# Kernel tuning notes

Hardware: AMD Instinct MI355X
Metric: run time of the kernel (lower is better)

The kernel has to match this reference:

```python
import jax, jax.numpy as jnp
import numpy as np

INPUT_DIM, HIDDEN, OUTPUT_DIM, NUM_LAYERS = 512, 128, 96, 5
BATCH, SEQ = 64, 512


def _gru_layer(x_seq, w_ih, w_hh, b_ih, b_hh):
    """Single GRU layer, PyTorch gate conventions. x_seq: [B,T,I] -> [B,T,H]."""
    B = x_seq.shape[0]
    H = w_hh.shape[1]
    # Precompute input-to-hidden gates for all timesteps: [B,T,3H]
    gx = jnp.einsum('bti,gi->btg', x_seq, w_ih) + b_ih

    def step(h, gx_t):
        gh = h @ w_hh.T + b_hh                      # [B,3H]
        xr, xz, xn = jnp.split(gx_t, 3, axis=-1)
        hr, hz, hn = jnp.split(gh, 3, axis=-1)
        r = jax.nn.sigmoid(xr + hr)
        z = jax.nn.sigmoid(xz + hz)
        n = jnp.tanh(xn + r * hn)
        h_new = (1.0 - z) * n + z * h
        return h_new, h_new

    h0 = jnp.zeros((B, H), x_seq.dtype)
    _, hs = jax.lax.scan(step, h0, jnp.swapaxes(gx, 0, 1))  # [T,B,H]
    return jnp.swapaxes(hs, 0, 1)                           # [B,T,H]


def setup_inputs() -> dict:
    key = jax.random.key(0)
    ks = jax.random.split(key, 8)
    s = 1.0 / np.sqrt(HIDDEN)  # torch default uniform init bound
    u = lambda k, shape: jax.random.uniform(k, shape, jnp.float32, -s, s)
    return {
        'x': jax.random.normal(ks[0], (BATCH, SEQ, INPUT_DIM), jnp.float32),
        'w_ih0': u(ks[1], (3 * HIDDEN, INPUT_DIM)),
        'w_ih_rest': u(ks[2], (NUM_LAYERS - 1, 3 * HIDDEN, HIDDEN)),
        'w_hh': u(ks[3], (NUM_LAYERS, 3 * HIDDEN, HIDDEN)),
        'b_ih': u(ks[4], (NUM_LAYERS, 3 * HIDDEN)),
        'b_hh': u(ks[5], (NUM_LAYERS, 3 * HIDDEN)),
        'fc_w': u(ks[6], (OUTPUT_DIM, HIDDEN)),
        'fc_b': u(ks[7], (OUTPUT_DIM,)),
    }


def reference(x, w_ih0, w_ih_rest, w_hh, b_ih, b_hh, fc_w, fc_b):
    h = _gru_layer(x, w_ih0, w_hh[0], b_ih[0], b_hh[0])
    for l in range(1, NUM_LAYERS):
        h = _gru_layer(h, w_ih_rest[l - 1], w_hh[l], b_ih[l], b_hh[l])
    # final linear on last timestep: [B,H] -> [B,OUTPUT_DIM]
    return h[:, -1, :] @ fc_w.T + fc_b
```

## Files before the change

kernel.cpp:

```cpp
#include <hip/hip_runtime.h>
#include <hip/hip_bf16.h>

#define BATCH   64
#define SEQ     512
#define IN0     512
#define HID     128
#define G3      384
#define NLAY    5
#define CHUNK   8

typedef _Float16 f16x8 __attribute__((ext_vector_type(8)));
typedef float    f32x4 __attribute__((ext_vector_type(4)));

static __device__ __forceinline__ float sigf(float x) {
    return __builtin_amdgcn_rcpf(1.f + __expf(-x));
}
static __device__ __forceinline__ float tanh_fast(float x) {
    const float e = __expf(-2.f * fabsf(x));
    return copysignf((1.f - e) * __builtin_amdgcn_rcpf(1.f + e), x);
}

__global__ __launch_bounds__(256) void gemm_gx(const float* __restrict__ A,
                                               const float* __restrict__ W,
                                               const float* __restrict__ bias,
                                               float* __restrict__ gx)
{
    __shared__ __align__(16) _Float16 As[64][40];
    __shared__ __align__(16) _Float16 Bs[64][40];

    const int tid  = threadIdx.x;
    const int lane = tid & 63;
    const int wv   = tid >> 6;
    const int n16  = lane & 15;
    const int quad = lane >> 4;
    const int row0 = blockIdx.x * 64;
    const int col0 = blockIdx.y * 64;
    const int r    = tid >> 2;
    const int kc   = (tid & 3) * 8;

    f32x4 acc[4];
    #pragma unroll
    for (int nt = 0; nt < 4; nt++) acc[nt] = (f32x4){0.f, 0.f, 0.f, 0.f};

    for (int k0 = 0; k0 < IN0; k0 += 32) {
        {
            const float* Ap = A + (size_t)(row0 + r) * IN0 + k0 + kc;
            float4 a0 = *(const float4*)(Ap);
            float4 a1 = *(const float4*)(Ap + 4);
            f16x8 v;
            v[0] = (_Float16)a0.x; v[1] = (_Float16)a0.y; v[2] = (_Float16)a0.z; v[3] = (_Float16)a0.w;
            v[4] = (_Float16)a1.x; v[5] = (_Float16)a1.y; v[6] = (_Float16)a1.z; v[7] = (_Float16)a1.w;
            *(f16x8*)&As[r][kc] = v;
        }
        {
            const float* Wp = W + (size_t)(col0 + r) * IN0 + k0 + kc;
            float4 b0 = *(const float4*)(Wp);
            float4 b1 = *(const float4*)(Wp + 4);
            f16x8 v;
            v[0] = (_Float16)b0.x; v[1] = (_Float16)b0.y; v[2] = (_Float16)b0.z; v[3] = (_Float16)b0.w;
            v[4] = (_Float16)b1.x; v[5] = (_Float16)b1.y; v[6] = (_Float16)b1.z; v[7] = (_Float16)b1.w;
            *(f16x8*)&Bs[r][kc] = v;
        }
        __syncthreads();

        const f16x8 af = *(const f16x8*)&As[wv * 16 + n16][quad * 8];
        #pragma unroll
        for (int nt = 0; nt < 4; nt++) {
            const f16x8 bfr = *(const f16x8*)&Bs[nt * 16 + n16][quad * 8];
            acc[nt] = __builtin_amdgcn_mfma_f32_16x16x32_f16(af, bfr, acc[nt], 0, 0, 0);
        }
        __syncthreads();
    }

    #pragma unroll
    for (int nt = 0; nt < 4; nt++) {
        const int col = col0 + nt * 16 + n16;
        const float bb = bias[col];
        #pragma unroll
        for (int r4 = 0; r4 < 4; r4++) {
            const int row = row0 + wv * 16 + quad * 4 + r4;
            gx[(size_t)row * G3 + col] = acc[nt][r4] + bb;
        }
    }
}

__global__ __launch_bounds__(512, 2) void gru_pipeline(
    const float* __restrict__ gx0,
    const float* __restrict__ w_ih_rest,
    const float* __restrict__ w_hh,
    const float* __restrict__ b_ih,
    const float* __restrict__ b_hh,
    _Float16* __restrict__ hmid,
    float* __restrict__ hlast,
    int* __restrict__ flags)
{
    const int l    = blockIdx.x >> 2;
    const int g    = blockIdx.x & 3;
    const int bm0  = g * 16;
    const int tid  = threadIdx.x;
    const int lane = tid & 63;
    const int n16  = lane & 15;
    const int quad = lane >> 4;
    const int wv   = tid >> 6;
    const int j    = wv * 16 + n16;

    __shared__ __align__(16) _Float16 hA[2][16][136];
    __shared__ int barcnt;

    f16x8 bf[3][4];
    {
        const float* wb = w_hh + (size_t)l * G3 * HID;
        #pragma unroll
        for (int tau = 0; tau < 3; tau++)
            #pragma unroll
            for (int kc = 0; kc < 4; kc++) {
                const float* wp = wb + (size_t)(tau * 128 + j) * HID + kc * 32 + quad * 8;
                f16x8 v;
                #pragma unroll
                for (int i = 0; i < 8; i++) v[i] = (_Float16)wp[i];
                bf[tau][kc] = v;
            }
    }
    f16x8 bi[3][4];
    if (l > 0) {
        const float* wb = w_ih_rest + (size_t)(l - 1) * G3 * HID;
        #pragma unroll
        for (int tau = 0; tau < 3; tau++)
            #pragma unroll
            for (int kc = 0; kc < 4; kc++) {
                const float* wp = wb + (size_t)(tau * 128 + j) * HID + kc * 32 + quad * 8;
                f16x8 v;
                #pragma unroll
                for (int i = 0; i < 8; i++) v[i] = (_Float16)wp[i];
                bi[tau][kc] = v;
            }
    }
    const float bcr = b_hh[l * G3 + j]       + ((l > 0) ? b_ih[l * G3 + j]       : 0.f);
    const float bcz = b_hh[l * G3 + j + 128] + ((l > 0) ? b_ih[l * G3 + j + 128] : 0.f);
    const float bcn = b_hh[l * G3 + j + 256];
    const float bxn = (l > 0) ? b_ih[l * G3 + j + 256] : 0.f;

    for (int i = tid; i < 2 * 16 * 136; i += 512) ((_Float16*)hA)[i] = (_Float16)0.f;
    float vhp[4] = {0.f, 0.f, 0.f, 0.f};
    if (tid == 0) barcnt = 0;

    const float* pR[4];
    float xr[4], xz[4], xn[4];
    if (l == 0) {
        #pragma unroll
        for (int r = 0; r < 4; r++) {
            pR[r] = gx0 + (size_t)(bm0 + quad * 4 + r) * SEQ * G3 + j;
            xr[r] = pR[r][0]; xz[r] = pR[r][128]; xn[r] = pR[r][256];
            pR[r] += G3;
        }
    }

    const _Float16* hprev = (l > 0) ? hmid + (size_t)((l - 1) * 4 + g) * SEQ * 2048 : (const _Float16*)nullptr;
    _Float16*       hpub  = (l < 4) ? hmid + (size_t)(l * 4 + g) * SEQ * 2048 : (_Float16*)nullptr;
    int*       dstflag = (l < 4) ? &flags[l * 4 + g] : (int*)nullptr;
    const int* srcflag = (l > 0) ? &flags[(l - 1) * 4 + g] : (const int*)nullptr;

    _Float16* hw = (l < 4) ? hpub + quad * 4 * 128 + j : (_Float16*)nullptr;

    f16x8 ap[4];
    const int hoff = n16 * 128 + quad * 8;

    __syncthreads();

    volatile int* bc = &barcnt;
    int btarget = 0;

    for (int c = 0; c < SEQ / CHUNK; c++) {
        const int t0 = c * CHUNK;

        if (l > 0) {
            const int need = t0 + CHUNK;
            int v = __hip_atomic_load(srcflag, __ATOMIC_RELAXED, __HIP_MEMORY_SCOPE_AGENT);
            while (v < need) {
                __builtin_amdgcn_s_sleep(2);
                v = __hip_atomic_load(srcflag, __ATOMIC_RELAXED, __HIP_MEMORY_SCOPE_AGENT);
            }
            (void)__hip_atomic_load(srcflag, __ATOMIC_ACQUIRE, __HIP_MEMORY_SCOPE_AGENT);
            __asm__ volatile("" ::: "memory");
            const _Float16* hp = hprev + (size_t)t0 * 2048 + hoff;
            #pragma unroll
            for (int kc = 0; kc < 4; kc++) ap[kc] = *(const f16x8*)(hp + kc * 32);
        }

        #pragma unroll
        for (int i = 0; i < CHUNK; i++) {
            const int t = t0 + i;

            __asm__ volatile("" ::: "memory");
            if (lane == 0) atomicAdd(&barcnt, 1);
            btarget += 8;
            while (*bc < btarget) { __builtin_amdgcn_s_sleep(1); }
            __asm__ volatile("" ::: "memory");

            const int buf = t & 1;
            f16x8 af[4];
            #pragma unroll
            for (int kc = 0; kc < 4; kc++)
                af[kc] = *(const f16x8*)&hA[buf][n16][kc * 32 + quad * 8];

            f32x4 ai0 = {0.f,0.f,0.f,0.f}, ai1 = ai0, ai2 = ai0;
            if (l > 0) {
                #pragma unroll
                for (int kc = 0; kc < 4; kc++) {
                    ai0 = __builtin_amdgcn_mfma_f32_16x16x32_f16(ap[kc], bi[0][kc], ai0, 0, 0, 0);
                    ai1 = __builtin_amdgcn_mfma_f32_16x16x32_f16(ap[kc], bi[1][kc], ai1, 0, 0, 0);
                    ai2 = __builtin_amdgcn_mfma_f32_16x16x32_f16(ap[kc], bi[2][kc], ai2, 0, 0, 0);
                }
            }
            float nr[4], nz[4], nn[4];
            if (l == 0) {
                #pragma unroll
                for (int r = 0; r < 4; r++) {
                    nr[r] = pR[r][0]; nz[r] = pR[r][128]; nn[r] = pR[r][256];
                }
                if (t + 1 < SEQ) {
                    #pragma unroll
                    for (int r = 0; r < 4; r++) pR[r] += G3;
                }
            }

            f32x4 ah0 = {0.f,0.f,0.f,0.f}, ah1 = ah0, ah2 = ah0;
            #pragma unroll
            for (int kc = 0; kc < 4; kc++) {
                ah0 = __builtin_amdgcn_mfma_f32_16x16x32_f16(af[kc], bf[0][kc], ah0, 0, 0, 0);
                ah1 = __builtin_amdgcn_mfma_f32_16x16x32_f16(af[kc], bf[1][kc], ah1, 0, 0, 0);
                ah2 = __builtin_amdgcn_mfma_f32_16x16x32_f16(af[kc], bf[2][kc], ah2, 0, 0, 0);
            }

            const int nbuf = buf ^ 1;
            #pragma unroll
            for (int r = 0; r < 4; r++) {
                const float sxr = (l == 0) ? xr[r] : ai0[r];
                const float sxz = (l == 0) ? xz[r] : ai1[r];
                const float sxn = ((l == 0) ? xn[r] : ai2[r]) + bxn;
                const float rg  = sigf(sxr + ah0[r] + bcr);
                const float zg  = sigf(sxz + ah1[r] + bcz);
                const float th  = tanh_fast(sxn + rg * (ah2[r] + bcn));
                const float hnew = fmaf(zg, vhp[r] - th, th);
                vhp[r] = hnew;
                hA[nbuf][quad * 4 + r][j] = (_Float16)hnew;
                if (l < 4) hw[r * 128] = (_Float16)hnew;
                if (l == 4 && t == SEQ - 1)
                    hlast[(bm0 + quad * 4 + r) * 128 + j] = hnew;
            }
            if (l < 4) hw += 2048;

            if (l == 0) {
                #pragma unroll
                for (int r = 0; r < 4; r++) { xr[r] = nr[r]; xz[r] = nz[r]; xn[r] = nn[r]; }
            }

            if (l > 0 && i < CHUNK - 1) {
                const _Float16* hp = hprev + (size_t)(t + 1) * 2048 + hoff;
                #pragma unroll
                for (int kc = 0; kc < 4; kc++) ap[kc] = *(const f16x8*)(hp + kc * 32);
            }
        }

        __syncthreads();
        if (l < 4 && tid == 0)
            __hip_atomic_store(dstflag, t0 + CHUNK, __ATOMIC_RELEASE, __HIP_MEMORY_SCOPE_AGENT);
    }
}

__global__ __launch_bounds__(128) void fc_kernel(const float* __restrict__ hlast,
                                                 const float* __restrict__ fc_w,
                                                 const float* __restrict__ fc_b,
                                                 float* __restrict__ out)
{
    const int b = blockIdx.x;
    const int o = threadIdx.x;
    if (o < 96) {
        const float* h = hlast + (size_t)b * HID;
        const float* wrow = fc_w + o * HID;
        float acc = fc_b[o];
        #pragma unroll 4
        for (int k = 0; k < HID; k++) acc = fmaf(h[k], wrow[k], acc);
        out[b * 96 + o] = acc;
    }
}

extern "C" void kernel_launch(void* const* d_in, const int* in_sizes, int n_in,
                              void* d_out, int out_size, void* d_ws, size_t ws_size,
                              hipStream_t stream)
{
    const float* x         = (const float*)d_in[0];
    const float* w_ih0     = (const float*)d_in[1];
    const float* w_ih_rest = (const float*)d_in[2];
    const float* w_hh      = (const float*)d_in[3];
    const float* b_ih      = (const float*)d_in[4];
    const float* b_hh      = (const float*)d_in[5];
    const float* fc_w      = (const float*)d_in[6];
    const float* fc_b      = (const float*)d_in[7];
    float* out = (float*)d_out;

    int*      flags = (int*)d_ws;
    float*    gxbuf = (float*)((char*)d_ws + 256);
    _Float16* hmid  = (_Float16*)((char*)d_ws + 256 + 50331648);
    float*    hlast = (float*)((char*)d_ws + 256 + 50331648 + 33554432);

    hipMemsetAsync(d_ws, 0, 256, stream);

    const dim3 gemmGrid(512, 6);
    gemm_gx<<<gemmGrid, 256, 0, stream>>>(x, w_ih0, b_ih, gxbuf);

    gru_pipeline<<<NLAY * 4, 512, 0, stream>>>(gxbuf, w_ih_rest, w_hh, b_ih, b_hh,
                                               hmid, hlast, flags);

    fc_kernel<<<BATCH, 128, 0, stream>>>(hlast, fc_w, fc_b, out);
}
```

Baseline: 983.9 us.

## Fuse layer-0 input GEMM into GRU kernel with per-chunk readiness counters

Merges the separate input-projection GEMM into the persistent GRU pipeline launch. Extra blocks compute gx tiles ordered by time chunk and batch group, then bump per-(group, time-chunk) counters. Layer-0 recurrent blocks spin on those counters before consuming each 128-step chunk. The goal is to overlap the GEMM with the start of the recurrence and drop one launch boundary. In exchange it relies on block scheduling order for forward progress, and the stores use relaxed ordering with no release fence before the counter increment.

```diff
diff --git a/kernel.cpp b/kernel.cpp
--- a/kernel.cpp
+++ b/kernel.cpp
@@ -20,88 +20,93 @@
     return copysignf((1.f - e) * __builtin_amdgcn_rcpf(1.f + e), x);
 }
 
-__global__ __launch_bounds__(256) void gemm_gx(const float* __restrict__ A,
-                                               const float* __restrict__ W,
-                                               const float* __restrict__ bias,
-                                               float* __restrict__ gx)
-{
-    __shared__ __align__(16) _Float16 As[64][40];
-    __shared__ __align__(16) _Float16 Bs[64][40];
-
-    const int tid  = threadIdx.x;
-    const int lane = tid & 63;
-    const int wv   = tid >> 6;
-    const int n16  = lane & 15;
-    const int quad = lane >> 4;
-    const int row0 = blockIdx.x * 64;
-    const int col0 = blockIdx.y * 64;
-    const int r    = tid >> 2;
-    const int kc   = (tid & 3) * 8;
-
-    f32x4 acc[4];
-    #pragma unroll
-    for (int nt = 0; nt < 4; nt++) acc[nt] = (f32x4){0.f, 0.f, 0.f, 0.f};
-
-    for (int k0 = 0; k0 < IN0; k0 += 32) {
-        {
-            const float* Ap = A + (size_t)(row0 + r) * IN0 + k0 + kc;
-            float4 a0 = *(const float4*)(Ap);
-            float4 a1 = *(const float4*)(Ap + 4);
-            f16x8 v;
-            v[0] = (_Float16)a0.x; v[1] = (_Float16)a0.y; v[2] = (_Float16)a0.z; v[3] = (_Float16)a0.w;
-            v[4] = (_Float16)a1.x; v[5] = (_Float16)a1.y; v[6] = (_Float16)a1.z; v[7] = (_Float16)a1.w;
-            *(f16x8*)&As[r][kc] = v;
-        }
-        {
-            const float* Wp = W + (size_t)(col0 + r) * IN0 + k0 + kc;
-            float4 b0 = *(const float4*)(Wp);
-            float4 b1 = *(const float4*)(Wp + 4);
-            f16x8 v;
-            v[0] = (_Float16)b0.x; v[1] = (_Float16)b0.y; v[2] = (_Float16)b0.z; v[3] = (_Float16)b0.w;
-            v[4] = (_Float16)b1.x; v[5] = (_Float16)b1.y; v[6] = (_Float16)b1.z; v[7] = (_Float16)b1.w;
-            *(f16x8*)&Bs[r][kc] = v;
-        }
-        __syncthreads();
-
-        const f16x8 af = *(const f16x8*)&As[wv * 16 + n16][quad * 8];
-        #pragma unroll
-        for (int nt = 0; nt < 4; nt++) {
-            const f16x8 bfr = *(const f16x8*)&Bs[nt * 16 + n16][quad * 8];
-            acc[nt] = __builtin_amdgcn_mfma_f32_16x16x32_f16(af, bfr, acc[nt], 0, 0, 0);
-        }
-        __syncthreads();
-    }
-
-    #pragma unroll
-    for (int nt = 0; nt < 4; nt++) {
-        const int col = col0 + nt * 16 + n16;
-        const float bb = bias[col];
-        #pragma unroll
-        for (int r4 = 0; r4 < 4; r4++) {
-            const int row = row0 + wv * 16 + quad * 4 + r4;
-            gx[(size_t)row * G3 + col] = acc[nt][r4] + bb;
-        }
-    }
-}
-
-__global__ __launch_bounds__(512, 2) void gru_pipeline(
-    const float* __restrict__ gx0,
+__global__ __launch_bounds__(512, 2) void gru_fused(
+    const float* __restrict__ x,
+    const float* __restrict__ w_ih0,
     const float* __restrict__ w_ih_rest,
     const float* __restrict__ w_hh,
     const float* __restrict__ b_ih,
     const float* __restrict__ b_hh,
+    float* __restrict__ gx0,
     _Float16* __restrict__ hmid,
     float* __restrict__ hlast,
-    int* __restrict__ flags)
+    int* __restrict__ flags,
+    int* __restrict__ gxcnt)
 {
-    const int l    = blockIdx.x >> 2;
-    const int g    = blockIdx.x & 3;
-    const int bm0  = g * 16;
     const int tid  = threadIdx.x;
     const int lane = tid & 63;
     const int n16  = lane & 15;
     const int quad = lane >> 4;
     const int wv   = tid >> 6;
+
+    if (blockIdx.x >= 20) {
+        __shared__ __align__(16) _Float16 As[128][40];
+        __shared__ __align__(16) _Float16 Bs[64][40];
+
+        const int gid   = blockIdx.x - 20;
+        const int q     = gid / 6;
+        const int ntile = gid % 6;
+        const int tc    = q >> 6;
+        const int b     = q & 63;
+        const int mt    = b * 4 + tc;
+        const int row0  = mt * 128;
+        const int col0  = ntile * 64;
+        const int ar    = tid >> 2;
+        const int kc    = (tid & 3) * 8;
+
+        f32x4 acc[4];
+        #pragma unroll
+        for (int nt = 0; nt < 4; nt++) acc[nt] = (f32x4){0.f, 0.f, 0.f, 0.f};
+
+        for (int k0 = 0; k0 < IN0; k0 += 32) {
+            {
+                const float* Ap = x + (size_t)(row0 + ar) * IN0 + k0 + kc;
+                float4 a0 = *(const float4*)(Ap);
+                float4 a1 = *(const float4*)(Ap + 4);
+                f16x8 v;
+                v[0] = (_Float16)a0.x; v[1] = (_Float16)a0.y; v[2] = (_Float16)a0.z; v[3] = (_Float16)a0.w;
+                v[4] = (_Float16)a1.x; v[5] = (_Float16)a1.y; v[6] = (_Float16)a1.z; v[7] = (_Float16)a1.w;
+                *(f16x8*)&As[ar][kc] = v;
+            }
+            if (tid < 256) {
+                const float* Wp = w_ih0 + (size_t)(col0 + (tid >> 2)) * IN0 + k0 + kc;
+                float4 b0 = *(const float4*)(Wp);
+                float4 b1 = *(const float4*)(Wp + 4);
+                f16x8 v;
+                v[0] = (_Float16)b0.x; v[1] = (_Float16)b0.y; v[2] = (_Float16)b0.z; v[3] = (_Float16)b0.w;
+                v[4] = (_Float16)b1.x; v[5] = (_Float16)b1.y; v[6] = (_Float16)b1.z; v[7] = (_Float16)b1.w;
+                *(f16x8*)&Bs[tid >> 2][kc] = v;
+            }
+            __syncthreads();
+
+            const f16x8 af = *(const f16x8*)&As[wv * 16 + n16][quad * 8];
+            #pragma unroll
+            for (int nt = 0; nt < 4; nt++) {
+                const f16x8 bfr = *(const f16x8*)&Bs[nt * 16 + n16][quad * 8];
+                acc[nt] = __builtin_amdgcn_mfma_f32_16x16x32_f16(af, bfr, acc[nt], 0, 0, 0);
+            }
+            __syncthreads();
+        }
+
+        #pragma unroll
+        for (int nt = 0; nt < 4; nt++) {
+            const int col = col0 + nt * 16 + n16;
+            const float bb = b_ih[col];
+            #pragma unroll
+            for (int r4 = 0; r4 < 4; r4++) {
+                const int row = row0 + wv * 16 + quad * 4 + r4;
+                __hip_atomic_store(&gx0[(size_t)row * G3 + col], acc[nt][r4] + bb,
+                                   __ATOMIC_RELAXED, __HIP_MEMORY_SCOPE_AGENT);
+            }
+        }
+        __syncthreads();
+        if (tid == 0) atomicAdd(&gxcnt[(mt >> 6) * 4 + (mt & 3)], 1);
+        return;
+    }
+
+    const int l    = blockIdx.x >> 2;
+    const int g    = blockIdx.x & 3;
+    const int bm0  = g * 16;
     const int j    = wv * 16 + n16;
 
     __shared__ __align__(16) _Float16 hA[2][16][136];
@@ -143,10 +148,19 @@
     for (int i = tid; i < 2 * 16 * 136; i += 512) ((_Float16*)hA)[i] = (_Float16)0.f;
     float vhp[4] = {0.f, 0.f, 0.f, 0.f};
     if (tid == 0) barcnt = 0;
+    __syncthreads();
 
     const float* pR[4];
     float xr[4], xz[4], xn[4];
+    int tcdone = 0;
     if (l == 0) {
+        int v = __hip_atomic_load(&gxcnt[g * 4], __ATOMIC_RELAXED, __HIP_MEMORY_SCOPE_AGENT);
+        while (v < 96) {
+            __builtin_amdgcn_s_sleep(8);
+            v = __hip_atomic_load(&gxcnt[g * 4], __ATOMIC_RELAXED, __HIP_MEMORY_SCOPE_AGENT);
+        }
+        __asm__ volatile("" ::: "memory");
+        tcdone = 1;
         #pragma unroll
         for (int r = 0; r < 4; r++) {
             pR[r] = gx0 + (size_t)(bm0 + quad * 4 + r) * SEQ * G3 + j;
@@ -164,8 +178,6 @@
 
     f16x8 ap[4];
     const int hoff = n16 * 128 + quad * 8;
-
-    __syncthreads();
 
     volatile int* bc = &barcnt;
     int btarget = 0;
@@ -185,6 +197,18 @@
             const _Float16* hp = hprev + (size_t)t0 * 2048 + hoff;
             #pragma unroll
             for (int kc = 0; kc < 4; kc++) ap[kc] = *(const f16x8*)(hp + kc * 32);
+        } else {
+            const int tneed = (t0 + CHUNK < SEQ) ? (t0 + CHUNK) : (SEQ - 1);
+            const int tc = tneed >> 7;
+            if (tc >= tcdone) {
+                int v = __hip_atomic_load(&gxcnt[g * 4 + tc], __ATOMIC_RELAXED, __HIP_MEMORY_SCOPE_AGENT);
+                while (v < 96) {
+                    __builtin_amdgcn_s_sleep(2);
+                    v = __hip_atomic_load(&gxcnt[g * 4 + tc], __ATOMIC_RELAXED, __HIP_MEMORY_SCOPE_AGENT);
+                }
+                __asm__ volatile("" ::: "memory");
+                tcdone = tc + 1;
+            }
         }
 
         #pragma unroll
@@ -300,17 +324,15 @@
     float* out = (float*)d_out;
 
     int*      flags = (int*)d_ws;
+    int*      gxcnt = (int*)d_ws + 16;
     float*    gxbuf = (float*)((char*)d_ws + 256);
     _Float16* hmid  = (_Float16*)((char*)d_ws + 256 + 50331648);
     float*    hlast = (float*)((char*)d_ws + 256 + 50331648 + 33554432);
 
     hipMemsetAsync(d_ws, 0, 256, stream);
 
-    const dim3 gemmGrid(512, 6);
-    gemm_gx<<<gemmGrid, 256, 0, stream>>>(x, w_ih0, b_ih, gxbuf);
-
-    gru_pipeline<<<NLAY * 4, 512, 0, stream>>>(gxbuf, w_ih_rest, w_hh, b_ih, b_hh,
-                                               hmid, hlast, flags);
+    gru_fused<<<20 + 1536, 512, 0, stream>>>(x, w_ih0, w_ih_rest, w_hh, b_ih, b_hh,
+                                             gxbuf, hmid, hlast, flags, gxcnt);
 
     fc_kernel<<<BATCH, 128, 0, stream>>>(hlast, fc_w, fc_b, out);
 }
```

Result: no change. 989.1 us (+0.5%).
